# Performance work log

Hardware: AMD Instinct MI355X
Metric: run time of the kernel (lower is better)

The kernel has to match this reference:

```python
import jax, jax.numpy as jnp
import numpy as np

NUM_Q = 8
DIM = 256
N_EMBED = 1024
COMMITMENT = 1.0


def setup_inputs() -> dict:
    key = jax.random.key(0)
    kx, ke = jax.random.split(key)
    x = jax.random.normal(kx, (32, 2048, DIM), dtype=jnp.float32)
    # one codebook per residual layer, stored as [dim, n_embed] like torch buffer `embed`
    embeds = jax.random.normal(ke, (NUM_Q, DIM, N_EMBED), dtype=jnp.float32)
    return {"x": x, "embeds": embeds}


def _vq_layer(residual, embed):
    # residual: [B, T, D]; embed: [D, K]
    flat = residual.reshape(-1, DIM)                                   # [N, D]
    dist = (jnp.sum(flat * flat, axis=1, keepdims=True)
            - 2.0 * flat @ embed
            + jnp.sum(embed * embed, axis=0, keepdims=True))           # [N, K]
    ind = jnp.argmin(dist, axis=1)                                     # [N]
    quantize = jnp.take(embed.T, ind, axis=0).reshape(residual.shape)  # [B, T, D]
    # commitment loss: mse(stopgrad(quantize), input)
    loss = jnp.mean((jax.lax.stop_gradient(quantize) - residual) ** 2) * COMMITMENT
    # straight-through estimator
    quantize_st = residual + jax.lax.stop_gradient(quantize - residual)
    # perplexity from code usage histogram
    counts = jnp.zeros((N_EMBED,), dtype=flat.dtype).at[ind].add(1.0)
    avg_probs = counts / flat.shape[0]
    perplexity = jnp.exp(-jnp.sum(avg_probs * jnp.log(avg_probs + 1e-10)))
    return quantize_st, loss, perplexity


def reference(x, embeds):
    def step(carry, embed):
        residual, quantized_out = carry
        q, loss, perp = _vq_layer(residual, embed)
        return (residual - q, quantized_out + q), (loss, perp)

    init = (x, jnp.zeros_like(x))
    (residual, quantized_out), (losses, perps) = jax.lax.scan(step, init, embeds)
    return quantized_out, losses, perps
```

## Files before the change

kernel.cpp:

```cpp
#include <hip/hip_runtime.h>
#include <math.h>
#include <stdint.h>

#define NQ 8
#define DIMV 256
#define KCODES 1024
#define NTOK 65536
#define NELEM (NTOK * DIMV)
#define TOKPB 64

typedef _Float16 f16x8 __attribute__((ext_vector_type(8)));
typedef float    f32x16 __attribute__((ext_vector_type(16)));

__device__ __forceinline__ int rotl3(int s) { return ((s << 3) | (s >> 2)) & 31; }

__global__ __launch_bounds__(256)
void vq_transpose(const float* __restrict__ embeds, float* __restrict__ embedT) {
    const int idx = blockIdx.x * 256 + threadIdx.x;
    const int q   = idx >> 18;
    const int rem = idx & 262143;
    const int k   = rem >> 8;
    const int d   = rem & 255;
    embedT[idx] = embeds[q * 262144 + d * 1024 + k];
}

__global__ __launch_bounds__(256)
void vq_e2(const float* __restrict__ embeds, float* __restrict__ e2) {
    const int idx = blockIdx.x * 256 + threadIdx.x;
    const int q = idx >> 10;
    const int k = idx & 1023;
    const float* e = embeds + q * 262144 + k;
    float s = 0.f;
    for (int d = 0; d < DIMV; ++d) {
        const float v = e[d * 1024];
        s += v * v;
    }
    e2[idx] = s;
}

__global__ __launch_bounds__(256)
void vq_embedB(const float* __restrict__ embeds, _Float16* __restrict__ embedB) {
    const int idx = blockIdx.x * 256 + threadIdx.x;
    const int j    = idx & 7;
    const int s    = (idx >> 3) & 127;
    const int part = (idx >> 10) & 1;
    const int w    = (idx >> 11) & 15;
    const int c    = (idx >> 15) & 15;
    const int q    = idx >> 19;
    const int h  = s >> 6;
    const int cl = s & 63;
    const int d  = c * 16 + h * 8 + j;
    const int k  = w * 64 + cl;
    const float v = embeds[q * 262144 + d * 1024 + k];
    const _Float16 hi = (_Float16)v;
    embedB[idx] = (part == 0) ? hi : (_Float16)(v - (float)hi);
}

#define LDS_BYTES 78272

__global__ __launch_bounds__(1024, 4)
void vq_fused(const float* __restrict__ x, float* __restrict__ out,
              const float* __restrict__ embedT, const float* __restrict__ e2,
              const _Float16* __restrict__ embedB,
              float* __restrict__ lossSum, int* __restrict__ counts) {
    extern __shared__ char smem[];
    _Float16* Ahi = (_Float16*)smem;
    _Float16* Alo = (_Float16*)(smem + 32768);
    float* bestS   = (float*)(smem + 65536);
    int*   bestI   = (int*)(smem + 69696);
    int*   indF    = (int*)(smem + 73856);
    float* lossRed = (float*)(smem + 74112);
    float* e2Lds   = (float*)(smem + 74176);

    const int tid    = threadIdx.x;
    const int wave   = tid >> 6;
    const int lane   = tid & 63;
    const int l32    = lane & 31;
    const int h32    = lane >> 5;
    const int tok0   = blockIdx.x * TOKPB;
    const int codeBase = wave * 64;

#pragma unroll
    for (int k = 0; k < 2; ++k) {
        const int si = tid + k * 1024;
        const int t  = si >> 5;
        const int s  = si & 31;
        const float4 v0 = *(const float4*)(x + (tok0 + t) * 256 + s * 8);
        const float4 v1 = *(const float4*)(x + (tok0 + t) * 256 + s * 8 + 4);
        const float vv[8] = {v0.x, v0.y, v0.z, v0.w, v1.x, v1.y, v1.z, v1.w};
        f16x8 h8, l8;
#pragma unroll
        for (int e = 0; e < 8; ++e) {
            const _Float16 hi = (_Float16)vv[e];
            h8[e] = hi;
            l8[e] = (_Float16)(vv[e] - (float)hi);
        }
        const int ss = rotl3(s) ^ (t & 31);
        ((f16x8*)(Ahi + t * 256))[ss] = h8;
        ((f16x8*)(Alo + t * 256))[ss] = l8;
    }

#pragma unroll 1
    for (int q = 0; q < NQ; ++q) {
        const _Float16* embedBq = embedB + q * 524288;
        const float*    embedTq = embedT + q * (KCODES * DIMV);

        e2Lds[tid] = e2[q * KCODES + tid];
        __syncthreads();

        const char* gBw = (const char*)embedBq + wave * 4096 + h32 * 1024 + l32 * 16;

        float bsv0 = 3.4e38f, bsv1 = 3.4e38f;
        int   biv0 = 0x7fffffff, biv1 = 0x7fffffff;

#pragma unroll
        for (int pass = 0; pass < 2; ++pass) {
            f32x16 acc[2];
#pragma unroll
            for (int tt = 0; tt < 2; ++tt)
#pragma unroll
                for (int r = 0; r < 16; ++r) acc[tt][r] = 0.f;

            const char* gBp = gBw + pass * 512;

            f16x8 bH[3], bL[3];
            bH[0] = *(const f16x8*)(gBp);
            bL[0] = *(const f16x8*)(gBp + 2048);
            bH[1] = *(const f16x8*)(gBp + 65536);
            bL[1] = *(const f16x8*)(gBp + 65536 + 2048);

#pragma unroll
            for (int c = 0; c < 16; ++c) {
                const int cs = c % 3;
                if (c < 14) {
                    const char* gBn = gBp + (c + 2) * 65536;
                    bH[(c + 2) % 3] = *(const f16x8*)(gBn);
                    bL[(c + 2) % 3] = *(const f16x8*)(gBn + 2048);
                }
                f16x8 aH[2], aL[2];
#pragma unroll
                for (int tt = 0; tt < 2; ++tt) {
                    const int t  = tt * 32 + l32;
                    const int ss = rotl3(2 * c + h32) ^ l32;
                    aH[tt] = ((const f16x8*)(Ahi + t * 256))[ss];
                    aL[tt] = ((const f16x8*)(Alo + t * 256))[ss];
                }
#pragma unroll
                for (int tt = 0; tt < 2; ++tt) {
                    acc[tt] = __builtin_amdgcn_mfma_f32_32x32x16_f16(
                        bH[cs], aH[tt], acc[tt], 0, 0, 0);
                    acc[tt] = __builtin_amdgcn_mfma_f32_32x32x16_f16(
                        bL[cs], aH[tt], acc[tt], 0, 0, 0);
                    acc[tt] = __builtin_amdgcn_mfma_f32_32x32x16_f16(
                        bH[cs], aL[tt], acc[tt], 0, 0, 0);
                }
            }

#pragma unroll
            for (int tt = 0; tt < 2; ++tt) {
                float bs = (tt == 0) ? bsv0 : bsv1;
                int   bi = (tt == 0) ? biv0 : biv1;
#pragma unroll
                for (int r = 0; r < 16; ++r) {
                    const int cd = codeBase + pass * 32 + (r & 3) + 8 * (r >> 2) + 4 * h32;
                    const float sc = e2Lds[cd] - 2.0f * acc[tt][r];
                    if (sc < bs || (sc == bs && cd < bi)) { bs = sc; bi = cd; }
                }
                if (tt == 0) { bsv0 = bs; biv0 = bi; } else { bsv1 = bs; biv1 = bi; }
            }
        }

#pragma unroll
        for (int tt = 0; tt < 2; ++tt) {
            float bs = (tt == 0) ? bsv0 : bsv1;
            int   bi = (tt == 0) ? biv0 : biv1;
            const float so = __shfl_xor(bs, 32);
            const int   io = __shfl_xor(bi, 32);
            if (so < bs || (so == bs && io < bi)) { bs = so; bi = io; }
            if (h32 == 0) {
                bestS[wave * 65 + tt * 32 + l32] = bs;
                bestI[wave * 65 + tt * 32 + l32] = bi;
            }
        }
        __syncthreads();

        if (tid < 256) {
            const int t = tid >> 2;
            const int g = tid & 3;
            float bs = 3.4e38f;
            int   bi = 0x7fffffff;
#pragma unroll
            for (int i = 0; i < 4; ++i) {
                const int w = g * 4 + i;
                const float s2 = bestS[w * 65 + t];
                const int   i2 = bestI[w * 65 + t];
                if (s2 < bs || (s2 == bs && i2 < bi)) { bs = s2; bi = i2; }
            }
#pragma unroll
            for (int m = 1; m < 4; m <<= 1) {
                const float so = __shfl_xor(bs, m);
                const int   io = __shfl_xor(bi, m);
                if (so < bs || (so == bs && io < bi)) { bs = so; bi = io; }
            }
            if (g == 0) {
                indF[t] = bi;
                atomicAdd(&counts[q * KCODES + bi], 1);
            }
        }
        __syncthreads();

        {
            const int tl = tid >> 4;
            const int sg = tid & 15;
            const int csel = indF[tl];
            const float* gq = embedTq + csel * 256 + sg * 16;
            float lp = 0.f;
            f16x8* rowH = (f16x8*)(Ahi + tl * 256);
            f16x8* rowL = (f16x8*)(Alo + tl * 256);
#pragma unroll
            for (int it = 0; it < 2; ++it) {
                const int slot = rotl3(sg * 2 + it) ^ (tl & 31);
                f16x8 h8 = rowH[slot];
                f16x8 l8 = rowL[slot];
                const float4 q0 = *(const float4*)(gq + it * 8);
                const float4 q1 = *(const float4*)(gq + it * 8 + 4);
                const float qv[8] = {q0.x, q0.y, q0.z, q0.w, q1.x, q1.y, q1.z, q1.w};
#pragma unroll
                for (int e = 0; e < 8; ++e) {
                    const float rv = (float)h8[e] + (float)l8[e];
                    const float nr = rv - qv[e];
                    lp += nr * nr;
                    const _Float16 nh = (_Float16)nr;
                    h8[e] = nh;
                    l8[e] = (_Float16)(nr - (float)nh);
                }
                rowH[slot] = h8;
                rowL[slot] = l8;
            }
#pragma unroll
            for (int off = 32; off > 0; off >>= 1) lp += __shfl_down(lp, off);
            if (lane == 0) lossRed[wave] = lp;
        }
        __syncthreads();
        if (tid < 64) {
            float v = (lane < 16) ? lossRed[lane] : 0.f;
#pragma unroll
            for (int off = 8; off > 0; off >>= 1) v += __shfl_down(v, off);
            if (lane == 0) atomicAdd(lossSum + q, v);
        }
    }

#pragma unroll
    for (int k = 0; k < 2; ++k) {
        const int si = tid + k * 1024;
        const int t  = si >> 5;
        const int s  = si & 31;
        const int ss = rotl3(s) ^ (t & 31);
        const f16x8 h8 = ((const f16x8*)(Ahi + t * 256))[ss];
        const f16x8 l8 = ((const f16x8*)(Alo + t * 256))[ss];
        const float4 x0 = *(const float4*)(x + (tok0 + t) * 256 + s * 8);
        const float4 x1 = *(const float4*)(x + (tok0 + t) * 256 + s * 8 + 4);
        float4 o0, o1;
        o0.x = x0.x - ((float)h8[0] + (float)l8[0]);
        o0.y = x0.y - ((float)h8[1] + (float)l8[1]);
        o0.z = x0.z - ((float)h8[2] + (float)l8[2]);
        o0.w = x0.w - ((float)h8[3] + (float)l8[3]);
        o1.x = x1.x - ((float)h8[4] + (float)l8[4]);
        o1.y = x1.y - ((float)h8[5] + (float)l8[5]);
        o1.z = x1.z - ((float)h8[6] + (float)l8[6]);
        o1.w = x1.w - ((float)h8[7] + (float)l8[7]);
        *(float4*)(out + (tok0 + t) * 256 + s * 8)     = o0;
        *(float4*)(out + (tok0 + t) * 256 + s * 8 + 4) = o1;
    }
}

__global__ __launch_bounds__(256)
void vq_finalize(const int* __restrict__ counts, const float* __restrict__ lossSum,
                 float* __restrict__ outTail) {
    const int q = blockIdx.x;
    const int tid = threadIdx.x;
    float s = 0.f;
    for (int k = tid; k < KCODES; k += 256) {
        const float p = (float)counts[q * KCODES + k] * (1.0f / 65536.0f);
        s += p * logf(p + 1e-10f);
    }
    for (int off = 32; off > 0; off >>= 1) s += __shfl_down(s, off);
    __shared__ float wpart[4];
    if ((tid & 63) == 0) wpart[tid >> 6] = s;
    __syncthreads();
    if (tid == 0) {
        outTail[q]     = lossSum[q] * (1.0f / 16777216.0f);
        outTail[8 + q] = expf(-(wpart[0] + wpart[1] + wpart[2] + wpart[3]));
    }
}

extern "C" void kernel_launch(void* const* d_in, const int* in_sizes, int n_in,
                              void* d_out, int out_size, void* d_ws, size_t ws_size,
                              hipStream_t stream) {
    const float* x      = (const float*)d_in[0];
    const float* embeds = (const float*)d_in[1];
    float* out = (float*)d_out;

    float* embedT   = (float*)d_ws;
    float* e2       = embedT + 2097152;
    float* lossSum  = e2 + 8192;
    int*   counts   = (int*)(lossSum + 8);
    _Float16* embedB = (_Float16*)(counts + 8192);

    hipMemsetAsync(lossSum, 0, (8 + 8192) * sizeof(float), stream);

    vq_transpose<<<8192, 256, 0, stream>>>(embeds, embedT);
    vq_e2<<<32, 256, 0, stream>>>(embeds, e2);
    vq_embedB<<<16384, 256, 0, stream>>>(embeds, embedB);

    hipFuncSetAttribute((const void*)vq_fused,
                        hipFuncAttributeMaxDynamicSharedMemorySize, LDS_BYTES);
    vq_fused<<<NTOK / TOKPB, 1024, LDS_BYTES, stream>>>(
        x, out, embedT, e2, embedB, lossSum, counts);

    vq_finalize<<<NQ, 256, 0, stream>>>(counts, lossSum, out + NELEM);
}
```

Baseline: 1.379 ms.

## Halve fused VQ block to 8 waves, each covering 128 codes

The fused kernel now launches 512 threads per block instead of 1024. Each wave computes distances for 128 codebook entries over four passes rather than 64 over two, and the staging, update and reduction loops are rewritten for the smaller thread count. This cuts the cross-wave argmin reduction and the barrier cost per block, and the smaller LDS footprint may allow more blocks per CU. In exchange each wave does twice the MFMA work serially, and there are fewer waves available to hide the global loads of codebook fragments.

```diff
diff --git a/kernel.cpp b/kernel.cpp
--- a/kernel.cpp
+++ b/kernel.cpp
@@ -56,9 +56,9 @@
     embedB[idx] = (part == 0) ? hi : (_Float16)(v - (float)hi);
 }
 
-#define LDS_BYTES 78272
-
-__global__ __launch_bounds__(1024, 4)
+#define LDS_BYTES 74080
+
+__global__ __launch_bounds__(512, 4)
 void vq_fused(const float* __restrict__ x, float* __restrict__ out,
               const float* __restrict__ embedT, const float* __restrict__ e2,
               const _Float16* __restrict__ embedB,
@@ -67,10 +67,10 @@
     _Float16* Ahi = (_Float16*)smem;
     _Float16* Alo = (_Float16*)(smem + 32768);
     float* bestS   = (float*)(smem + 65536);
-    int*   bestI   = (int*)(smem + 69696);
-    int*   indF    = (int*)(smem + 73856);
-    float* lossRed = (float*)(smem + 74112);
-    float* e2Lds   = (float*)(smem + 74176);
+    int*   bestI   = (int*)(smem + 67616);
+    int*   indF    = (int*)(smem + 69696);
+    float* lossRed = (float*)(smem + 69952);
+    float* e2Lds   = (float*)(smem + 69984);
 
     const int tid    = threadIdx.x;
     const int wave   = tid >> 6;
@@ -78,11 +78,10 @@
     const int l32    = lane & 31;
     const int h32    = lane >> 5;
     const int tok0   = blockIdx.x * TOKPB;
-    const int codeBase = wave * 64;
-
-#pragma unroll
-    for (int k = 0; k < 2; ++k) {
-        const int si = tid + k * 1024;
+
+#pragma unroll
+    for (int k = 0; k < 4; ++k) {
+        const int si = tid + k * 512;
         const int t  = si >> 5;
         const int s  = si & 31;
         const float4 v0 = *(const float4*)(x + (tok0 + t) * 256 + s * 8);
@@ -105,23 +104,23 @@
         const _Float16* embedBq = embedB + q * 524288;
         const float*    embedTq = embedT + q * (KCODES * DIMV);
 
-        e2Lds[tid] = e2[q * KCODES + tid];
+        e2Lds[tid]       = e2[q * KCODES + tid];
+        e2Lds[tid + 512] = e2[q * KCODES + tid + 512];
         __syncthreads();
-
-        const char* gBw = (const char*)embedBq + wave * 4096 + h32 * 1024 + l32 * 16;
 
         float bsv0 = 3.4e38f, bsv1 = 3.4e38f;
         int   biv0 = 0x7fffffff, biv1 = 0x7fffffff;
 
 #pragma unroll
-        for (int pass = 0; pass < 2; ++pass) {
+        for (int p = 0; p < 4; ++p) {
             f32x16 acc[2];
 #pragma unroll
             for (int tt = 0; tt < 2; ++tt)
 #pragma unroll
                 for (int r = 0; r < 16; ++r) acc[tt][r] = 0.f;
 
-            const char* gBp = gBw + pass * 512;
+            const char* gBp = (const char*)embedBq + (2 * wave + (p >> 1)) * 4096
+                              + (p & 1) * 512 + h32 * 1024 + l32 * 16;
 
             f16x8 bH[3], bL[3];
             bH[0] = *(const f16x8*)(gBp);
@@ -162,7 +161,7 @@
                 int   bi = (tt == 0) ? biv0 : biv1;
 #pragma unroll
                 for (int r = 0; r < 16; ++r) {
-                    const int cd = codeBase + pass * 32 + (r & 3) + 8 * (r >> 2) + 4 * h32;
+                    const int cd = wave * 128 + p * 32 + (r & 3) + 8 * (r >> 2) + 4 * h32;
                     const float sc = e2Lds[cd] - 2.0f * acc[tt][r];
                     if (sc < bs || (sc == bs && cd < bi)) { bs = sc; bi = cd; }
                 }
@@ -184,20 +183,13 @@
         }
         __syncthreads();
 
-        if (tid < 256) {
-            const int t = tid >> 2;
-            const int g = tid & 3;
-            float bs = 3.4e38f;
-            int   bi = 0x7fffffff;
-#pragma unroll
-            for (int i = 0; i < 4; ++i) {
-                const int w = g * 4 + i;
-                const float s2 = bestS[w * 65 + t];
-                const int   i2 = bestI[w * 65 + t];
-                if (s2 < bs || (s2 == bs && i2 < bi)) { bs = s2; bi = i2; }
-            }
-#pragma unroll
-            for (int m = 1; m < 4; m <<= 1) {
+        {
+            const int t = tid >> 3;
+            const int g = tid & 7;
+            float bs = bestS[g * 65 + t];
+            int   bi = bestI[g * 65 + t];
+#pragma unroll
+            for (int m = 1; m < 8; m <<= 1) {
                 const float so = __shfl_xor(bs, m);
                 const int   io = __shfl_xor(bi, m);
                 if (so < bs || (so == bs && io < bi)) { bs = so; bi = io; }
@@ -210,20 +202,21 @@
         __syncthreads();
 
         {
-            const int tl = tid >> 4;
-            const int sg = tid & 15;
+            const int tl = tid >> 3;
+            const int sg = tid & 7;
             const int csel = indF[tl];
-            const float* gq = embedTq + csel * 256 + sg * 16;
+            const float* gq = embedTq + csel * 256;
             float lp = 0.f;
             f16x8* rowH = (f16x8*)(Ahi + tl * 256);
             f16x8* rowL = (f16x8*)(Alo + tl * 256);
 #pragma unroll
-            for (int it = 0; it < 2; ++it) {
-                const int slot = rotl3(sg * 2 + it) ^ (tl & 31);
+            for (int it = 0; it < 4; ++it) {
+                const int slotIdx = sg * 4 + it;
+                const int slot = rotl3(slotIdx) ^ (tl & 31);
                 f16x8 h8 = rowH[slot];
                 f16x8 l8 = rowL[slot];
-                const float4 q0 = *(const float4*)(gq + it * 8);
-                const float4 q1 = *(const float4*)(gq + it * 8 + 4);
+                const float4 q0 = *(const float4*)(gq + slotIdx * 8);
+                const float4 q1 = *(const float4*)(gq + slotIdx * 8 + 4);
                 const float qv[8] = {q0.x, q0.y, q0.z, q0.w, q1.x, q1.y, q1.z, q1.w};
 #pragma unroll
                 for (int e = 0; e < 8; ++e) {
@@ -243,16 +236,16 @@
         }
         __syncthreads();
         if (tid < 64) {
-            float v = (lane < 16) ? lossRed[lane] : 0.f;
-#pragma unroll
-            for (int off = 8; off > 0; off >>= 1) v += __shfl_down(v, off);
+            float v = (lane < 8) ? lossRed[lane] : 0.f;
+#pragma unroll
+            for (int off = 4; off > 0; off >>= 1) v += __shfl_down(v, off);
             if (lane == 0) atomicAdd(lossSum + q, v);
         }
     }
 
 #pragma unroll
-    for (int k = 0; k < 2; ++k) {
-        const int si = tid + k * 1024;
+    for (int k = 0; k < 4; ++k) {
+        const int si = tid + k * 512;
         const int t  = si >> 5;
         const int s  = si & 31;
         const int ss = rotl3(s) ^ (t & 31);
@@ -315,7 +308,7 @@
 
     hipFuncSetAttribute((const void*)vq_fused,
                         hipFuncAttributeMaxDynamicSharedMemorySize, LDS_BYTES);
-    vq_fused<<<NTOK / TOKPB, 1024, LDS_BYTES, stream>>>(
+    vq_fused<<<NTOK / TOKPB, 512, LDS_BYTES, stream>>>(
         x, out, embedT, e2, embedB, lossSum, counts);
 
     vq_finalize<<<NQ, 256, 0, stream>>>(counts, lossSum, out + NELEM);
```

After: 1.189 ms. -13.8%, faster.
